# Kernel tuning notes

Measured on AMD Instinct MI355X. Metric: run time of the kernel, lower is better.

## Reference

```python
import jax, jax.numpy as jnp
import numpy as np

DIM = 512
HEADS = 8
DHEAD = 64
B, H, W = 4, 128, 128


def _dwconv(x, k):
    # x: (b, c, h, w), k: (c, 1, 3, 3) depthwise kernel (groups = c)
    return jax.lax.conv_general_dilated(
        x, k, window_strides=(1, 1), padding='SAME',
        dimension_numbers=('NCHW', 'OIHW', 'NCHW'),
        feature_group_count=x.shape[1])


def _l2norm(x, eps=1e-12):
    # torch F.normalize(p=2, dim=-1): x / clamp(||x||, eps)
    n = jnp.sqrt(jnp.sum(x * x, axis=-1, keepdims=True))
    return x / jnp.maximum(n, eps)


def setup_inputs() -> dict:
    key = jax.random.key(0)
    ks = jax.random.split(key, 10)
    s = 0.02
    return {
        'x_in': jax.random.normal(ks[0], (B, H, W, DIM), jnp.float32),
        'illu_fea_trans': jax.random.uniform(ks[1], (B, H, W, DIM), jnp.float32),
        'Wq': jax.random.normal(ks[2], (DIM, DIM), jnp.float32) * s,  # (out,in), no bias
        'Wk': jax.random.normal(ks[3], (DIM, DIM), jnp.float32) * s,
        'Wv': jax.random.normal(ks[4], (DIM, DIM), jnp.float32) * s,
        'rescale': jnp.ones((HEADS, 1, 1), jnp.float32),
        'Wp': jax.random.normal(ks[5], (DIM, DIM), jnp.float32) * s,  # proj weight (out,in)
        'bp': jnp.zeros((DIM,), jnp.float32),
        'pe1': jax.random.normal(ks[6], (DIM, 1, 3, 3), jnp.float32) * s,  # depthwise conv kernels
        'pe2': jax.random.normal(ks[7], (DIM, 1, 3, 3), jnp.float32) * s,
    }


def reference(x_in, illu_fea_trans, Wq, Wk, Wv, rescale, Wp, bp, pe1, pe2):
    b, h, w, c = x_in.shape
    n = h * w
    x = x_in.reshape(b, n, c)
    illu = illu_fea_trans.reshape(b, n, c)

    q = x @ Wq.T
    k = x @ Wk.T
    v = x @ Wv.T

    def to_heads_dn(t):  # (b, n, heads*d) -> (b, heads, d, n)
        return t.reshape(b, n, HEADS, DHEAD).transpose(0, 2, 3, 1)

    illu_h = illu.reshape(b, n, HEADS, DHEAD)
    v = ((v.reshape(b, n, HEADS, DHEAD)) * illu_h).transpose(0, 2, 3, 1)  # (b,heads,d,n)
    q = _l2norm(to_heads_dn(q))  # normalize along n
    k = _l2norm(to_heads_dn(k))

    # channel attention: (b,heads,d,d) score matrix
    attn = jnp.einsum('bhdn,bhen->bhde', k, q) * rescale
    attn = jax.nn.softmax(attn, axis=-1)
    xo = jnp.einsum('bhde,bhen->bhdn', attn, v)  # (b,heads,d,n)

    xo = xo.transpose(0, 3, 1, 2).reshape(b, n, HEADS * DHEAD)  # (b,n,c)
    out_c = (xo @ Wp.T + bp).reshape(b, h, w, c)

    # positional branch: depthwise conv -> GELU -> depthwise conv on v image
    v_img = v.reshape(b, HEADS * DHEAD, h, w)
    p = _dwconv(v_img, pe1)
    p = jax.nn.gelu(p, approximate=False)  # torch F.gelu default = erf
    p = _dwconv(p, pe2)
    out_p = p.transpose(0, 2, 3, 1)

    return out_c + out_p
```

## Files before the change

kernel.cpp:

```cpp
#include <hip/hip_runtime.h>
#include <hip/hip_bf16.h>
#include <math.h>

typedef __bf16 bf16;
typedef __attribute__((ext_vector_type(8))) __bf16 bf16x8;
typedef __attribute__((ext_vector_type(4))) float f32x4;

#define GLL(gp, lp) __builtin_amdgcn_global_load_lds( \
    (const __attribute__((address_space(1))) unsigned int*)(gp), \
    (__attribute__((address_space(3))) unsigned int*)(lp), 16, 0, 0)


__device__ __forceinline__ bf16x8 cvt8(float4 a, float4 b) {
  bf16x8 o;
  o[0] = (bf16)a.x; o[1] = (bf16)a.y; o[2] = (bf16)a.z; o[3] = (bf16)a.w;
  o[4] = (bf16)b.x; o[5] = (bf16)b.y; o[6] = (bf16)b.z; o[7] = (bf16)b.w;
  return o;
}

__global__ __launch_bounds__(256) void prep_kernel(
    const float* __restrict__ x, const float* __restrict__ Wq,
    const float* __restrict__ Wk, const float* __restrict__ Wv,
    bf16* __restrict__ xb, bf16* __restrict__ wqkv,
    float* __restrict__ zattn, float* __restrict__ ssq, float* __restrict__ ssk)
{
  const long XG = 33554432L / 8;
  const long WG = 262144L / 8;
  long i = (long)blockIdx.x * 256 + threadIdx.x;
  if (i < XG) {
    const float4* xp = (const float4*)x;
    float4 a = xp[i * 2], b = xp[i * 2 + 1];
    *(bf16x8*)(xb + i * 8) = cvt8(a, b);
  } else if (i < XG + 3 * WG) {
    long j = i - XG;
    int w = (int)(j / WG);
    long r = j % WG;
    const float* src = (w == 0) ? Wq : ((w == 1) ? Wk : Wv);
    const float4* sp = (const float4*)src;
    float4 a = sp[r * 2], b = sp[r * 2 + 1];
    *(bf16x8*)(wqkv + (long)w * 262144 + r * 8) = cvt8(a, b);
  } else {
    long j = (i - XG - 3 * WG) * 8;
    float4 z = make_float4(0.f, 0.f, 0.f, 0.f);
    if (j < 131072) {
      *(float4*)(zattn + j) = z; *(float4*)(zattn + j + 4) = z;
    } else if (j < 133120) {
      long r = j - 131072; *(float4*)(ssq + r) = z; *(float4*)(ssq + r + 4) = z;
    } else {
      long r = j - 133120; *(float4*)(ssk + r) = z; *(float4*)(ssk + r + 4) = z;
    }
  }
}

__device__ __forceinline__ void gemm_tile_mainloop(
    const bf16* __restrict__ A, const bf16* __restrict__ B,
    int m0, int n0, bf16* As, bf16* Bs, f32x4 acc[4][4])
{
  int tid = threadIdx.x;
  int lane = tid & 63, wave = tid >> 6;
  int wy = wave >> 1, wx = wave & 1;
  int srow = tid >> 3;
  int scol = ((tid & 7) ^ (srow & 7)) * 8;
  const bf16* ag = A + ((size_t)(m0 + srow) << 9) + scol;
  const bf16* bg = B + ((size_t)(n0 + srow) << 9) + scol;
  bf16* lA = As + wave * 512;
  bf16* lB = Bs + wave * 512;
  int mloc = lane & 15;
  int kq = lane >> 4;

#pragma unroll
  for (int i = 0; i < 4; i++) {
    GLL(ag + i * 16384, lA + i * 2048);
    GLL(bg + i * 16384, lB + i * 2048);
  }
  __syncthreads();

#pragma unroll
  for (int k0 = 0; k0 < 512; k0 += 64) {
    int cur = (k0 >> 6) & 1;
    if (k0 + 64 < 512) {
      int nb = cur ^ 1;
#pragma unroll
      for (int i = 0; i < 4; i++) {
        GLL(ag + (k0 + 64) + i * 16384, lA + nb * 8192 + i * 2048);
        GLL(bg + (k0 + 64) + i * 16384, lB + nb * 8192 + i * 2048);
      }
    }
    const bf16* Ac = As + (cur << 13);
    const bf16* Bc = Bs + (cur << 13);
#pragma unroll
    for (int kh = 0; kh < 2; kh++) {
      bf16x8 af[4], bfr[4];
      int logical = kh * 4 + kq;
#pragma unroll
      for (int tt = 0; tt < 4; tt++) {
        int arow = wy * 64 + tt * 16 + mloc;
        af[tt] = *(const bf16x8*)&Ac[arow * 64 + (logical ^ (arow & 7)) * 8];
        int brow = wx * 64 + tt * 16 + mloc;
        bfr[tt] = *(const bf16x8*)&Bc[brow * 64 + (logical ^ (brow & 7)) * 8];
      }
#pragma unroll
      for (int ty = 0; ty < 4; ty++)
#pragma unroll
        for (int tx = 0; tx < 4; tx++)
          acc[ty][tx] = __builtin_amdgcn_mfma_f32_16x16x32_bf16(
              af[ty], bfr[tx], acc[ty][tx], 0, 0, 0);
    }
    __syncthreads();
  }
}

__global__ __launch_bounds__(256) void gemm_qkv_kernel(
    const bf16* __restrict__ xb, const bf16* __restrict__ wqkv,
    const float* __restrict__ illu,
    bf16* __restrict__ qb, bf16* __restrict__ kb, bf16* __restrict__ vb,
    float* __restrict__ ssq, float* __restrict__ ssk)
{
  __shared__ __align__(16) bf16 As[16384];
  __shared__ __align__(16) bf16 Bs[16384];
  int bid = blockIdx.x;
  int xcd = bid & 7, s = bid >> 3;
  int mt = xcd * 64 + s / 12, nt = s % 12;
  int m0 = mt * 128, n0 = nt * 128;
  f32x4 acc[4][4] = {};
  gemm_tile_mainloop(xb, wqkv, m0, n0, As, Bs, acc);

  int tid = threadIdx.x, lane = tid & 63, wave = tid >> 6;
  int wy = wave >> 1, wx = wave & 1;
  int r0 = m0 + wy * 64 + ((lane >> 4) << 2);
  int c0 = n0 + wx * 64 + (lane & 15);
  int region = n0 >> 9;
  if (region < 2) {
    bf16* outp = region ? kb : qb;
    float* dst = (region ? ssk : ssq) + (m0 >> 14) * 512;
#pragma unroll
    for (int tx = 0; tx < 4; tx++) {
      int lc = (c0 + tx * 16) & 511;
      float ss = 0.f;
#pragma unroll
      for (int ty = 0; ty < 4; ty++) {
#pragma unroll
        for (int r = 0; r < 4; r++) {
          float v = acc[ty][tx][r];
          ss += v * v;
          outp[((size_t)(r0 + ty * 16 + r) << 9) + lc] = (bf16)v;
        }
      }
      ss += __shfl_xor(ss, 16);
      ss += __shfl_xor(ss, 32);
      if ((lane >> 4) == 0) atomicAdd(dst + lc, ss);
    }
  } else {
#pragma unroll
    for (int tx = 0; tx < 4; tx++) {
      int lc = (c0 + tx * 16) & 511;
#pragma unroll
      for (int ty = 0; ty < 4; ty++) {
#pragma unroll
        for (int r = 0; r < 4; r++) {
          size_t idx = ((size_t)(r0 + ty * 16 + r) << 9) + lc;
          vb[idx] = (bf16)(acc[ty][tx][r] * illu[idx]);
        }
      }
    }
  }
}

__global__ __launch_bounds__(256) void attn_dots_kernel(
    const bf16* __restrict__ qb, const bf16* __restrict__ kb,
    float* __restrict__ attn)
{
  __shared__ __align__(16) float ks[32 * 68];
  __shared__ __align__(16) float qs[32 * 68];
  int bh = blockIdx.x, sp = blockIdx.y;
  int b = bh >> 3, h = bh & 7;
  size_t hb = ((size_t)b << 23) + (size_t)h * 64;
  const bf16* qp = qb + hb;
  const bf16* kp = kb + hb;
  int t = threadIdx.x;
  int srow = t >> 3, scg = (t & 7) * 8;
  int d0 = (t & 15) * 4, e0 = (t >> 4) * 4;
  float acc[16] = {0};
  int nb = sp * 1024;
  for (int c = 0; c < 1024; c += 32) {
    size_t off = ((size_t)(nb + c + srow) << 9) + scg;
    bf16x8 kv = *(const bf16x8*)(kp + off);
    bf16x8 qv = *(const bf16x8*)(qp + off);
    __syncthreads();
    float* kd = &ks[srow * 68 + scg];
    float* qd = &qs[srow * 68 + scg];
#pragma unroll
    for (int i = 0; i < 8; i++) { kd[i] = (float)kv[i]; qd[i] = (float)qv[i]; }
    __syncthreads();
#pragma unroll 8
    for (int n = 0; n < 32; n++) {
      float4 kr = *(const float4*)&ks[n * 68 + d0];
      float4 qr = *(const float4*)&qs[n * 68 + e0];
      acc[0]  += kr.x * qr.x; acc[1]  += kr.x * qr.y; acc[2]  += kr.x * qr.z; acc[3]  += kr.x * qr.w;
      acc[4]  += kr.y * qr.x; acc[5]  += kr.y * qr.y; acc[6]  += kr.y * qr.z; acc[7]  += kr.y * qr.w;
      acc[8]  += kr.z * qr.x; acc[9]  += kr.z * qr.y; acc[10] += kr.z * qr.z; acc[11] += kr.z * qr.w;
      acc[12] += kr.w * qr.x; acc[13] += kr.w * qr.y; acc[14] += kr.w * qr.z; acc[15] += kr.w * qr.w;
    }
  }
  float* ap = attn + ((size_t)bh << 12);
#pragma unroll
  for (int i = 0; i < 4; i++)
#pragma unroll
    for (int j = 0; j < 4; j++)
      atomicAdd(&ap[(d0 + i) * 64 + (e0 + j)], acc[i * 4 + j]);
}

__global__ __launch_bounds__(64) void softmax_kernel(
    float* __restrict__ attn, const float* __restrict__ ssq,
    const float* __restrict__ ssk, const float* __restrict__ rescale)
{
  int bh = blockIdx.x, d = blockIdx.y;
  int b = bh >> 3, h = bh & 7;
  int e = threadIdx.x;
  float nq = fmaxf(sqrtf(ssq[b * 512 + h * 64 + e]), 1e-12f);
  float nk = fmaxf(sqrtf(ssk[b * 512 + h * 64 + d]), 1e-12f);
  float* ap = attn + ((size_t)bh << 12) + d * 64;
  float v = ap[e] * rescale[h] / (nk * nq);
  float m = v;
  for (int o = 32; o > 0; o >>= 1) m = fmaxf(m, __shfl_xor(m, o));
  float ex = expf(v - m);
  float s = ex;
  for (int o = 32; o > 0; o >>= 1) s += __shfl_xor(s, o);
  ap[e] = ex / s;
}

__global__ __launch_bounds__(256) void weff_kernel(
    const float* __restrict__ attn, const float* __restrict__ Wp,
    bf16* __restrict__ wefT)
{
  int cog = blockIdx.x, h = blockIdx.y, b = blockIdx.z;
  __shared__ float at[4096];
  __shared__ float wp[4096];
  int t = threadIdx.x;
  const float* ap = attn + ((size_t)(b * 8 + h) << 12);
  for (int i = t; i < 4096; i += 256) at[i] = ap[i];
  for (int i = t; i < 4096; i += 256) {
    int r = i >> 6, d = i & 63;
    wp[i] = Wp[((size_t)(cog * 64 + r) << 9) + h * 64 + d];
  }
  __syncthreads();
  int co_l = (t & 15) * 4, e_l = (t >> 4) * 4;
  float acc[16] = {0};
  for (int d = 0; d < 64; d++) {
    float w0 = wp[(co_l + 0) * 64 + d];
    float w1 = wp[(co_l + 1) * 64 + d];
    float w2 = wp[(co_l + 2) * 64 + d];
    float w3 = wp[(co_l + 3) * 64 + d];
    float4 av = *(const float4*)&at[d * 64 + e_l];
    acc[0]  += w0 * av.x; acc[1]  += w0 * av.y; acc[2]  += w0 * av.z; acc[3]  += w0 * av.w;
    acc[4]  += w1 * av.x; acc[5]  += w1 * av.y; acc[6]  += w1 * av.z; acc[7]  += w1 * av.w;
    acc[8]  += w2 * av.x; acc[9]  += w2 * av.y; acc[10] += w2 * av.z; acc[11] += w2 * av.w;
    acc[12] += w3 * av.x; acc[13] += w3 * av.y; acc[14] += w3 * av.z; acc[15] += w3 * av.w;
  }
#pragma unroll
  for (int i = 0; i < 4; i++)
#pragma unroll
    for (int j = 0; j < 4; j++)
      wefT[((size_t)b << 18) + ((size_t)(cog * 64 + co_l + i) << 9) + h * 64 + e_l + j] =
          (bf16)acc[i * 4 + j];
}

__global__ __launch_bounds__(256) void gemm_out_kernel(
    const bf16* __restrict__ vb, const bf16* __restrict__ wefT,
    const float* __restrict__ bp, float* __restrict__ out)
{
  __shared__ __align__(16) bf16 As[16384];
  __shared__ __align__(16) bf16 Bs[16384];
  int b = blockIdx.y;
  int bid = blockIdx.x;
  int xcd = bid & 7, s = bid >> 3;
  int mt = xcd * 16 + (s >> 2), nt = s & 3;
  int m0 = mt * 128, n0 = nt * 128;
  const bf16* A = vb + ((size_t)b << 23);
  const bf16* B = wefT + ((size_t)b << 18);
  f32x4 acc[4][4] = {};
  gemm_tile_mainloop(A, B, m0, n0, As, Bs, acc);

  int tid = threadIdx.x, lane = tid & 63, wave = tid >> 6;
  int wy = wave >> 1, wx = wave & 1;
  int r0 = (b << 14) + m0 + wy * 64 + ((lane >> 4) << 2);
  int c0 = n0 + wx * 64 + (lane & 15);
#pragma unroll
  for (int ty = 0; ty < 4; ty++) {
#pragma unroll
    for (int tx = 0; tx < 4; tx++) {
      int lc = c0 + tx * 16;
      float bias = bp[lc];
#pragma unroll
      for (int r = 0; r < 4; r++) {
        int grow = r0 + ty * 16 + r;
        out[((size_t)grow << 9) + lc] = acc[ty][tx][r] + bias;
      }
    }
  }
}

__global__ __launch_bounds__(256) void conv1_kernel(
    const bf16* __restrict__ vb, const float* __restrict__ pe1,
    bf16* __restrict__ pbuf)
{
  int b = blockIdx.y;
  int tile = blockIdx.x;
  int y0 = (tile >> 4) * 8, x0 = (tile & 15) * 8;
  int t = threadIdx.x;
  int cg = (t & 63) * 8, sp0 = t >> 6;
  float w[72];
#pragma unroll
  for (int i = 0; i < 8; i++)
#pragma unroll
    for (int k = 0; k < 9; k++)
      w[i * 9 + k] = pe1[(cg + i) * 9 + k];
  const bf16* vbase = vb + ((size_t)b << 23);
  bf16* pb = pbuf + ((size_t)b << 23);
  for (int s = sp0; s < 64; s += 4) {
    int y = y0 + (s >> 3), x = x0 + (s & 7);
    float a[8] = {0, 0, 0, 0, 0, 0, 0, 0};
#pragma unroll
    for (int ky = 0; ky < 3; ky++) {
      int yy = y + ky - 1;
      if (yy < 0 || yy >= 128) continue;
#pragma unroll
      for (int kx = 0; kx < 3; kx++) {
        int xx = x + kx - 1;
        if (xx < 0 || xx >= 128) continue;
        bf16x8 vv = *(const bf16x8*)&vbase[((size_t)(yy * 128 + xx) << 9) + cg];
#pragma unroll
        for (int i = 0; i < 8; i++) a[i] += (float)vv[i] * w[i * 9 + ky * 3 + kx];
      }
    }
    bf16x8 o;
#pragma unroll
    for (int i = 0; i < 8; i++) {
      float g = 0.5f * a[i] * (1.0f + erff(a[i] * 0.70710678118654752f));
      o[i] = (bf16)g;
    }
    *(bf16x8*)&pb[((size_t)(y * 128 + x) << 9) + cg] = o;
  }
}

__global__ __launch_bounds__(256) void conv2_kernel(
    const bf16* __restrict__ pbuf, const float* __restrict__ pe2,
    float* __restrict__ out)
{
  int b = blockIdx.y;
  int tile = blockIdx.x;
  int y0 = (tile >> 4) * 8, x0 = (tile & 15) * 8;
  int t = threadIdx.x;
  int cg = (t & 63) * 8, sp0 = t >> 6;
  float w[72];
#pragma unroll
  for (int i = 0; i < 8; i++)
#pragma unroll
    for (int k = 0; k < 9; k++)
      w[i * 9 + k] = pe2[(cg + i) * 9 + k];
  const bf16* pb = pbuf + ((size_t)b << 23);
  float* ob = out + ((size_t)b << 23);
  for (int s = sp0; s < 64; s += 4) {
    int y = y0 + (s >> 3), x = x0 + (s & 7);
    float a[8] = {0, 0, 0, 0, 0, 0, 0, 0};
#pragma unroll
    for (int ky = 0; ky < 3; ky++) {
      int yy = y + ky - 1;
      if (yy < 0 || yy >= 128) continue;
#pragma unroll
      for (int kx = 0; kx < 3; kx++) {
        int xx = x + kx - 1;
        if (xx < 0 || xx >= 128) continue;
        bf16x8 vv = *(const bf16x8*)&pb[((size_t)(yy * 128 + xx) << 9) + cg];
#pragma unroll
        for (int i = 0; i < 8; i++) a[i] += (float)vv[i] * w[i * 9 + ky * 3 + kx];
      }
    }
    size_t oi = ((size_t)(y * 128 + x) << 9) + cg;
    float4 o0 = *(float4*)&ob[oi];
    float4 o1 = *(float4*)&ob[oi + 4];
    o0.x += a[0]; o0.y += a[1]; o0.z += a[2]; o0.w += a[3];
    o1.x += a[4]; o1.y += a[5]; o1.z += a[6]; o1.w += a[7];
    *(float4*)&ob[oi] = o0;
    *(float4*)&ob[oi + 4] = o1;
  }
}

extern "C" void kernel_launch(void* const* d_in, const int* in_sizes, int n_in,
                              void* d_out, int out_size, void* d_ws, size_t ws_size,
                              hipStream_t stream) {
  (void)in_sizes; (void)n_in; (void)out_size; (void)ws_size;
  const float* x       = (const float*)d_in[0];
  const float* illu    = (const float*)d_in[1];
  const float* Wq      = (const float*)d_in[2];
  const float* Wk      = (const float*)d_in[3];
  const float* Wv      = (const float*)d_in[4];
  const float* rescale = (const float*)d_in[5];
  const float* Wp      = (const float*)d_in[6];
  const float* bp      = (const float*)d_in[7];
  const float* pe1     = (const float*)d_in[8];
  const float* pe2     = (const float*)d_in[9];
  float* out = (float*)d_out;
  char* ws = (char*)d_ws;

  bf16*  xb   = (bf16*)(ws);
  bf16*  wqkv = (bf16*)(ws + 67108864);
  bf16*  qb   = (bf16*)(ws + 68681728);
  bf16*  kb   = (bf16*)(ws + 135790592);
  bf16*  vb   = (bf16*)(ws + 202899456);
  float* ssq  = (float*)(ws + 270008320);
  float* ssk  = (float*)(ws + 270016512);
  float* attn = (float*)(ws + 270024704);
  bf16*  wefT = (bf16*)(ws + 270548992);
  bf16*  pbuf = xb;

  prep_kernel<<<16834, 256, 0, stream>>>(x, Wq, Wk, Wv, xb, wqkv, attn, ssq, ssk);
  gemm_qkv_kernel<<<6144, 256, 0, stream>>>(xb, wqkv, illu, qb, kb, vb, ssq, ssk);
  attn_dots_kernel<<<dim3(32, 16), 256, 0, stream>>>(qb, kb, attn);
  softmax_kernel<<<dim3(32, 64), 64, 0, stream>>>(attn, ssq, ssk, rescale);
  weff_kernel<<<dim3(8, 8, 4), 256, 0, stream>>>(attn, Wp, wefT);
  gemm_out_kernel<<<dim3(512, 4), 256, 0, stream>>>(vb, wefT, bp, out);
  conv1_kernel<<<dim3(256, 4), 256, 0, stream>>>(vb, pe1, pbuf);
  conv2_kernel<<<dim3(256, 4), 256, 0, stream>>>(pbuf, pe2, out);
}
```

Baseline: 838.3 us.

## Use 256x256 GEMM tiles with 8 waves and phased explicit-wait pipelining

Both bf16 GEMMs (QKV projection and output projection) move from 128x128 tiles with 4 waves to 256x256 tiles with 8 waves per block. The main loop is rewritten into four compute phases per k-step, with staggered global-to-LDS loads, explicit vmcnt/lgkmcnt waits, raw s_barrier and setprio around the MFMA bursts. The aim is higher arithmetic intensity per LDS byte and better overlap of loads with MFMA. In exchange LDS use per block doubles to 128KB, and register pressure rises to 32 accumulators per thread, which may limit occupancy or cause spills.

Result: slower. 940.6 us (+12.2%).

```diff
diff --git a/kernel.cpp b/kernel.cpp
--- a/kernel.cpp
+++ b/kernel.cpp
@@ -9,6 +9,12 @@
 #define GLL(gp, lp) __builtin_amdgcn_global_load_lds( \
     (const __attribute__((address_space(1))) unsigned int*)(gp), \
     (__attribute__((address_space(3))) unsigned int*)(lp), 16, 0, 0)
+
+#define S_BARRIER() __builtin_amdgcn_s_barrier()
+#define WAIT_LGKM0() do { asm volatile("s_waitcnt lgkmcnt(0)" ::: "memory"); \
+                          __builtin_amdgcn_sched_barrier(0); } while (0)
+#define WAIT_VMC(n) do { asm volatile("s_waitcnt vmcnt(" #n ")" ::: "memory"); \
+                         __builtin_amdgcn_sched_barrier(0); } while (0)
 
 
 __device__ __forceinline__ bf16x8 cvt8(float4 a, float4 b) {
@@ -52,98 +58,125 @@
   }
 }
 
-__device__ __forceinline__ void gemm_tile_mainloop(
+__device__ __forceinline__ void gemm256_mainloop(
     const bf16* __restrict__ A, const bf16* __restrict__ B,
-    int m0, int n0, bf16* As, bf16* Bs, f32x4 acc[4][4])
-{
-  int tid = threadIdx.x;
-  int lane = tid & 63, wave = tid >> 6;
-  int wy = wave >> 1, wx = wave & 1;
-  int srow = tid >> 3;
-  int scol = ((tid & 7) ^ (srow & 7)) * 8;
+    int m0, int n0, bf16* As, bf16* Bs, f32x4 (&acc)[8][4])
+{
+  const int tid = threadIdx.x;
+  const int lane = tid & 63, wave = tid >> 6;
+  const int wy = wave >> 2, wx = wave & 3;
+  const int srow = tid >> 3;
+  const int scol = ((tid & 7) ^ (srow & 7)) * 8;
   const bf16* ag = A + ((size_t)(m0 + srow) << 9) + scol;
   const bf16* bg = B + ((size_t)(n0 + srow) << 9) + scol;
   bf16* lA = As + wave * 512;
   bf16* lB = Bs + wave * 512;
-  int mloc = lane & 15;
-  int kq = lane >> 4;
-
-#pragma unroll
-  for (int i = 0; i < 4; i++) {
-    GLL(ag + i * 16384, lA + i * 2048);
-    GLL(bg + i * 16384, lB + i * 2048);
-  }
-  __syncthreads();
-
-#pragma unroll
-  for (int k0 = 0; k0 < 512; k0 += 64) {
-    int cur = (k0 >> 6) & 1;
-    if (k0 + 64 < 512) {
-      int nb = cur ^ 1;
-#pragma unroll
-      for (int i = 0; i < 4; i++) {
-        GLL(ag + (k0 + 64) + i * 16384, lA + nb * 8192 + i * 2048);
-        GLL(bg + (k0 + 64) + i * 16384, lB + nb * 8192 + i * 2048);
-      }
-    }
-    const bf16* Ac = As + (cur << 13);
-    const bf16* Bc = Bs + (cur << 13);
-#pragma unroll
-    for (int kh = 0; kh < 2; kh++) {
-      bf16x8 af[4], bfr[4];
-      int logical = kh * 4 + kq;
-#pragma unroll
-      for (int tt = 0; tt < 4; tt++) {
-        int arow = wy * 64 + tt * 16 + mloc;
-        af[tt] = *(const bf16x8*)&Ac[arow * 64 + (logical ^ (arow & 7)) * 8];
-        int brow = wx * 64 + tt * 16 + mloc;
-        bfr[tt] = *(const bf16x8*)&Bc[brow * 64 + (logical ^ (brow & 7)) * 8];
-      }
-#pragma unroll
-      for (int ty = 0; ty < 4; ty++)
-#pragma unroll
-        for (int tx = 0; tx < 4; tx++)
-          acc[ty][tx] = __builtin_amdgcn_mfma_f32_16x16x32_bf16(
-              af[ty], bfr[tx], acc[ty][tx], 0, 0, 0);
-    }
-    __syncthreads();
-  }
-}
-
-__global__ __launch_bounds__(256) void gemm_qkv_kernel(
+  const int mloc = lane & 15, kq = lane >> 4;
+
+#define STG_A(t, i) GLL(ag + (size_t)(i) * 32768 + (t) * 64, \
+                        lA + (((t) & 1) * 16384 + (i) * 4096))
+#define STG_B(t, i) GLL(bg + (size_t)(i) * 32768 + (t) * 64, \
+                        lB + (((t) & 1) * 16384 + (i) * 4096))
+
+#pragma unroll
+  for (int i = 0; i < 4; ++i) STG_A(0, i);
+#pragma unroll
+  for (int i = 0; i < 4; ++i) STG_B(0, i);
+#pragma unroll
+  for (int i = 0; i < 4; ++i) STG_B(1, i);
+  WAIT_VMC(4);
+  S_BARRIER();
+
+  bf16x8 af[4][2];
+  bf16x8 bfr[2][2][2];
+
+#pragma unroll
+  for (int kt = 0; kt < 8; ++kt) {
+    const int s = kt & 1;
+#pragma unroll
+    for (int ph = 0; ph < 4; ++ph) {
+      const int rh = ph >> 1, ch = ph & 1;
+      if (ch == 0) {
+#pragma unroll
+        for (int rt = 0; rt < 4; ++rt) {
+          const int r = wy * 128 + rh * 64 + rt * 16 + mloc;
+#pragma unroll
+          for (int kh = 0; kh < 2; ++kh)
+            af[rt][kh] = *(const bf16x8*)
+                &As[s * 16384 + r * 64 + (((kh * 4 + kq) ^ (r & 7)) << 3)];
+        }
+      }
+      if (ph < 2) {
+#pragma unroll
+        for (int ct = 0; ct < 2; ++ct) {
+          const int nr = wx * 64 + ch * 32 + ct * 16 + mloc;
+#pragma unroll
+          for (int kh = 0; kh < 2; ++kh)
+            bfr[ch][ct][kh] = *(const bf16x8*)
+                &Bs[s * 16384 + nr * 64 + (((kh * 4 + kq) ^ (nr & 7)) << 3)];
+        }
+      }
+      if (ph == 0 && kt + 1 < 8) { STG_A(kt + 1, 0); STG_A(kt + 1, 1); }
+      if (ph == 1 && kt + 1 < 8) { STG_A(kt + 1, 2); STG_A(kt + 1, 3); }
+      if (ph == 2 && kt + 2 < 8) { STG_B(kt + 2, 0); STG_B(kt + 2, 1); }
+      if (ph == 3 && kt + 2 < 8) { STG_B(kt + 2, 2); STG_B(kt + 2, 3); }
+      if (ph == 3) {
+        if (kt <= 5)      { WAIT_VMC(4); }
+        else if (kt == 6) { WAIT_VMC(0); }
+      }
+      S_BARRIER();
+      WAIT_LGKM0();
+      __builtin_amdgcn_s_setprio(1);
+#pragma unroll
+      for (int rt = 0; rt < 4; ++rt)
+#pragma unroll
+        for (int ct = 0; ct < 2; ++ct)
+#pragma unroll
+          for (int kh = 0; kh < 2; ++kh)
+            acc[rh * 4 + rt][ch * 2 + ct] = __builtin_amdgcn_mfma_f32_16x16x32_bf16(
+                af[rt][kh], bfr[ch][ct][kh], acc[rh * 4 + rt][ch * 2 + ct], 0, 0, 0);
+      __builtin_amdgcn_s_setprio(0);
+      S_BARRIER();
+    }
+  }
+#undef STG_A
+#undef STG_B
+}
+
+__global__ __launch_bounds__(512, 2) void gemm_qkv_kernel(
     const bf16* __restrict__ xb, const bf16* __restrict__ wqkv,
     const float* __restrict__ illu,
     bf16* __restrict__ qb, bf16* __restrict__ kb, bf16* __restrict__ vb,
     float* __restrict__ ssq, float* __restrict__ ssk)
 {
-  __shared__ __align__(16) bf16 As[16384];
-  __shared__ __align__(16) bf16 Bs[16384];
+  __shared__ __align__(16) bf16 As[32768];
+  __shared__ __align__(16) bf16 Bs[32768];
   int bid = blockIdx.x;
   int xcd = bid & 7, s = bid >> 3;
-  int mt = xcd * 64 + s / 12, nt = s % 12;
-  int m0 = mt * 128, n0 = nt * 128;
-  f32x4 acc[4][4] = {};
-  gemm_tile_mainloop(xb, wqkv, m0, n0, As, Bs, acc);
+  int mt = xcd * 32 + s / 6, nt = s % 6;
+  int m0 = mt * 256, n0 = nt * 256;
+  f32x4 acc[8][4] = {};
+  gemm256_mainloop(xb, wqkv, m0, n0, As, Bs, acc);
 
   int tid = threadIdx.x, lane = tid & 63, wave = tid >> 6;
-  int wy = wave >> 1, wx = wave & 1;
-  int r0 = m0 + wy * 64 + ((lane >> 4) << 2);
+  int wy = wave >> 2, wx = wave & 3;
+  int r0 = m0 + wy * 128 + ((lane >> 4) << 2);
   int c0 = n0 + wx * 64 + (lane & 15);
   int region = n0 >> 9;
   if (region < 2) {
     bf16* outp = region ? kb : qb;
     float* dst = (region ? ssk : ssq) + (m0 >> 14) * 512;
 #pragma unroll
-    for (int tx = 0; tx < 4; tx++) {
-      int lc = (c0 + tx * 16) & 511;
+    for (int tj = 0; tj < 4; ++tj) {
+      int lc = (c0 + tj * 16) & 511;
       float ss = 0.f;
 #pragma unroll
-      for (int ty = 0; ty < 4; ty++) {
-#pragma unroll
-        for (int r = 0; r < 4; r++) {
-          float v = acc[ty][tx][r];
+      for (int ti = 0; ti < 8; ++ti) {
+#pragma unroll
+        for (int r = 0; r < 4; ++r) {
+          float v = acc[ti][tj][r];
           ss += v * v;
-          outp[((size_t)(r0 + ty * 16 + r) << 9) + lc] = (bf16)v;
+          outp[((size_t)(r0 + ti * 16 + r) << 9) + lc] = (bf16)v;
         }
       }
       ss += __shfl_xor(ss, 16);
@@ -152,14 +185,14 @@
     }
   } else {
 #pragma unroll
-    for (int tx = 0; tx < 4; tx++) {
-      int lc = (c0 + tx * 16) & 511;
-#pragma unroll
-      for (int ty = 0; ty < 4; ty++) {
-#pragma unroll
-        for (int r = 0; r < 4; r++) {
-          size_t idx = ((size_t)(r0 + ty * 16 + r) << 9) + lc;
-          vb[idx] = (bf16)(acc[ty][tx][r] * illu[idx]);
+    for (int tj = 0; tj < 4; ++tj) {
+      int lc = (c0 + tj * 16) & 511;
+#pragma unroll
+      for (int ti = 0; ti < 8; ++ti) {
+#pragma unroll
+        for (int r = 0; r < 4; ++r) {
+          size_t idx = ((size_t)(r0 + ti * 16 + r) << 9) + lc;
+          vb[idx] = (bf16)(acc[ti][tj][r] * illu[idx]);
         }
       }
     }
@@ -265,36 +298,36 @@
           (bf16)acc[i * 4 + j];
 }
 
-__global__ __launch_bounds__(256) void gemm_out_kernel(
+__global__ __launch_bounds__(512, 2) void gemm_out_kernel(
     const bf16* __restrict__ vb, const bf16* __restrict__ wefT,
     const float* __restrict__ bp, float* __restrict__ out)
 {
-  __shared__ __align__(16) bf16 As[16384];
-  __shared__ __align__(16) bf16 Bs[16384];
+  __shared__ __align__(16) bf16 As[32768];
+  __shared__ __align__(16) bf16 Bs[32768];
   int b = blockIdx.y;
   int bid = blockIdx.x;
   int xcd = bid & 7, s = bid >> 3;
-  int mt = xcd * 16 + (s >> 2), nt = s & 3;
-  int m0 = mt * 128, n0 = nt * 128;
+  int mt = xcd * 8 + (s >> 1), nt = s & 1;
+  int m0 = mt * 256, n0 = nt * 256;
   const bf16* A = vb + ((size_t)b << 23);
   const bf16* B = wefT + ((size_t)b << 18);
-  f32x4 acc[4][4] = {};
-  gemm_tile_mainloop(A, B, m0, n0, As, Bs, acc);
+  f32x4 acc[8][4] = {};
+  gemm256_mainloop(A, B, m0, n0, As, Bs, acc);
 
   int tid = threadIdx.x, lane = tid & 63, wave = tid >> 6;
-  int wy = wave >> 1, wx = wave & 1;
-  int r0 = (b << 14) + m0 + wy * 64 + ((lane >> 4) << 2);
+  int wy = wave >> 2, wx = wave & 3;
+  int r0 = (b << 14) + m0 + wy * 128 + ((lane >> 4) << 2);
   int c0 = n0 + wx * 64 + (lane & 15);
 #pragma unroll
-  for (int ty = 0; ty < 4; ty++) {
-#pragma unroll
-    for (int tx = 0; tx < 4; tx++) {
-      int lc = c0 + tx * 16;
+  for (int ti = 0; ti < 8; ++ti) {
+#pragma unroll
+    for (int tj = 0; tj < 4; ++tj) {
+      int lc = c0 + tj * 16;
       float bias = bp[lc];
 #pragma unroll
-      for (int r = 0; r < 4; r++) {
-        int grow = r0 + ty * 16 + r;
-        out[((size_t)grow << 9) + lc] = acc[ty][tx][r] + bias;
+      for (int r = 0; r < 4; ++r) {
+        int grow = r0 + ti * 16 + r;
+        out[((size_t)grow << 9) + lc] = acc[ti][tj][r] + bias;
       }
     }
   }
@@ -415,11 +448,11 @@
   bf16*  pbuf = xb;
 
   prep_kernel<<<16834, 256, 0, stream>>>(x, Wq, Wk, Wv, xb, wqkv, attn, ssq, ssk);
-  gemm_qkv_kernel<<<6144, 256, 0, stream>>>(xb, wqkv, illu, qb, kb, vb, ssq, ssk);
+  gemm_qkv_kernel<<<1536, 512, 0, stream>>>(xb, wqkv, illu, qb, kb, vb, ssq, ssk);
   attn_dots_kernel<<<dim3(32, 16), 256, 0, stream>>>(qb, kb, attn);
   softmax_kernel<<<dim3(32, 64), 64, 0, stream>>>(attn, ssq, ssk, rescale);
   weff_kernel<<<dim3(8, 8, 4), 256, 0, stream>>>(attn, Wp, wefT);
-  gemm_out_kernel<<<dim3(512, 4), 256, 0, stream>>>(vb, wefT, bp, out);
+  gemm_out_kernel<<<dim3(128, 4), 512, 0, stream>>>(vb, wefT, bp, out);
   conv1_kernel<<<dim3(256, 4), 256, 0, stream>>>(vb, pe1, pbuf);
   conv2_kernel<<<dim3(256, 4), 256, 0, stream>>>(pbuf, pe2, out);
 }
```

## Store Q/K transposed and compute channel-attention dots with MFMA

Applied to the files above, without the earlier changes.

The QKV GEMM epilogue now writes Q and K in a channel-major (transposed) layout with 4-wide vector stores along n. The attn_dots kernel then streams contiguous n-chunks straight into swizzled LDS via global_load_lds and computes the 64x64 K·Q^T products with bf16 MFMA, each wave taking its own n slice, instead of scalar FP32 FMAs over LDS tiles. This removes the bf16-to-float conversion and the scalar inner loop, at the cost of more atomicAdds per block (one per wave) and strided transposed stores in the GEMM epilogue.

Result: faster. 810.7 us (-3.3%).

```diff
diff --git a/kernel.cpp b/kernel.cpp
--- a/kernel.cpp
+++ b/kernel.cpp
@@ -3,12 +3,18 @@
 #include <math.h>
 
 typedef __bf16 bf16;
+typedef __attribute__((ext_vector_type(4))) __bf16 bf16x4;
 typedef __attribute__((ext_vector_type(8))) __bf16 bf16x8;
 typedef __attribute__((ext_vector_type(4))) float f32x4;
 
 #define GLL(gp, lp) __builtin_amdgcn_global_load_lds( \
     (const __attribute__((address_space(1))) unsigned int*)(gp), \
     (__attribute__((address_space(3))) unsigned int*)(lp), 16, 0, 0)
+
+#define WAIT_LGKM0() do { asm volatile("s_waitcnt lgkmcnt(0)" ::: "memory"); \
+                          __builtin_amdgcn_sched_barrier(0); } while (0)
+#define WAIT_VMC0() do { asm volatile("s_waitcnt vmcnt(0)" ::: "memory"); \
+                         __builtin_amdgcn_sched_barrier(0); } while (0)
 
 
 __device__ __forceinline__ bf16x8 cvt8(float4 a, float4 b) {
@@ -113,7 +119,7 @@
 __global__ __launch_bounds__(256) void gemm_qkv_kernel(
     const bf16* __restrict__ xb, const bf16* __restrict__ wqkv,
     const float* __restrict__ illu,
-    bf16* __restrict__ qb, bf16* __restrict__ kb, bf16* __restrict__ vb,
+    bf16* __restrict__ qbT, bf16* __restrict__ kbT, bf16* __restrict__ vb,
     float* __restrict__ ssq, float* __restrict__ ssk)
 {
   __shared__ __align__(16) bf16 As[16384];
@@ -131,20 +137,22 @@
   int c0 = n0 + wx * 64 + (lane & 15);
   int region = n0 >> 9;
   if (region < 2) {
-    bf16* outp = region ? kb : qb;
+    bf16* outp = region ? kbT : qbT;
     float* dst = (region ? ssk : ssq) + (m0 >> 14) * 512;
+    int bb = r0 >> 14;
+    int nl0 = r0 & 16383;
 #pragma unroll
     for (int tx = 0; tx < 4; tx++) {
       int lc = (c0 + tx * 16) & 511;
+      bf16* colp = outp + (((size_t)bb << 23) + ((size_t)lc << 14));
       float ss = 0.f;
 #pragma unroll
       for (int ty = 0; ty < 4; ty++) {
-#pragma unroll
-        for (int r = 0; r < 4; r++) {
-          float v = acc[ty][tx][r];
-          ss += v * v;
-          outp[((size_t)(r0 + ty * 16 + r) << 9) + lc] = (bf16)v;
-        }
+        f32x4 a = acc[ty][tx];
+        ss += a[0] * a[0] + a[1] * a[1] + a[2] * a[2] + a[3] * a[3];
+        bf16x4 o;
+        o[0] = (bf16)a[0]; o[1] = (bf16)a[1]; o[2] = (bf16)a[2]; o[3] = (bf16)a[3];
+        *(bf16x4*)&colp[nl0 + ty * 16] = o;
       }
       ss += __shfl_xor(ss, 16);
       ss += __shfl_xor(ss, 32);
@@ -167,47 +175,62 @@
 }
 
 __global__ __launch_bounds__(256) void attn_dots_kernel(
-    const bf16* __restrict__ qb, const bf16* __restrict__ kb,
+    const bf16* __restrict__ qbT, const bf16* __restrict__ kbT,
     float* __restrict__ attn)
 {
-  __shared__ __align__(16) float ks[32 * 68];
-  __shared__ __align__(16) float qs[32 * 68];
+  __shared__ __align__(16) bf16 ks[4][4096];
+  __shared__ __align__(16) bf16 qs[4][4096];
   int bh = blockIdx.x, sp = blockIdx.y;
   int b = bh >> 3, h = bh & 7;
-  size_t hb = ((size_t)b << 23) + (size_t)h * 64;
-  const bf16* qp = qb + hb;
-  const bf16* kp = kb + hb;
-  int t = threadIdx.x;
-  int srow = t >> 3, scg = (t & 7) * 8;
-  int d0 = (t & 15) * 4, e0 = (t >> 4) * 4;
-  float acc[16] = {0};
-  int nb = sp * 1024;
-  for (int c = 0; c < 1024; c += 32) {
-    size_t off = ((size_t)(nb + c + srow) << 9) + scg;
-    bf16x8 kv = *(const bf16x8*)(kp + off);
-    bf16x8 qv = *(const bf16x8*)(qp + off);
-    __syncthreads();
-    float* kd = &ks[srow * 68 + scg];
-    float* qd = &qs[srow * 68 + scg];
-#pragma unroll
-    for (int i = 0; i < 8; i++) { kd[i] = (float)kv[i]; qd[i] = (float)qv[i]; }
-    __syncthreads();
-#pragma unroll 8
-    for (int n = 0; n < 32; n++) {
-      float4 kr = *(const float4*)&ks[n * 68 + d0];
-      float4 qr = *(const float4*)&qs[n * 68 + e0];
-      acc[0]  += kr.x * qr.x; acc[1]  += kr.x * qr.y; acc[2]  += kr.x * qr.z; acc[3]  += kr.x * qr.w;
-      acc[4]  += kr.y * qr.x; acc[5]  += kr.y * qr.y; acc[6]  += kr.y * qr.z; acc[7]  += kr.y * qr.w;
-      acc[8]  += kr.z * qr.x; acc[9]  += kr.z * qr.y; acc[10] += kr.z * qr.z; acc[11] += kr.z * qr.w;
-      acc[12] += kr.w * qr.x; acc[13] += kr.w * qr.y; acc[14] += kr.w * qr.z; acc[15] += kr.w * qr.w;
-    }
+  int t = threadIdx.x, lane = t & 63, w = t >> 6;
+  size_t base = ((size_t)b << 23) + ((size_t)h << 20);
+  int n0 = sp * 1024 + w * 256;
+  int srow = lane >> 3;
+  int scol = ((lane & 7) ^ (srow & 7)) << 3;
+  const bf16* kg = kbT + base + (size_t)srow * 16384 + n0 + scol;
+  const bf16* qg = qbT + base + (size_t)srow * 16384 + n0 + scol;
+  bf16* lk = &ks[w][0];
+  bf16* lq = &qs[w][0];
+  int mloc = lane & 15, kq = lane >> 4;
+  f32x4 acc[4][4] = {};
+
+  for (int it = 0; it < 4; ++it) {
+    WAIT_LGKM0();
+#pragma unroll
+    for (int i = 0; i < 8; ++i) {
+      GLL(kg + it * 64 + (size_t)i * 131072, lk + i * 512);
+      GLL(qg + it * 64 + (size_t)i * 131072, lq + i * 512);
+    }
+    WAIT_VMC0();
+    bf16x8 af[4][2], bfq[4][2];
+#pragma unroll
+    for (int tt = 0; tt < 4; ++tt) {
+      int r = tt * 16 + mloc;
+#pragma unroll
+      for (int kh = 0; kh < 2; ++kh) {
+        int slot = (kh * 4 + kq) ^ (r & 7);
+        af[tt][kh]  = *(const bf16x8*)&lk[r * 64 + slot * 8];
+        bfq[tt][kh] = *(const bf16x8*)&lq[r * 64 + slot * 8];
+      }
+    }
+#pragma unroll
+    for (int kh = 0; kh < 2; ++kh)
+#pragma unroll
+      for (int ta = 0; ta < 4; ++ta)
+#pragma unroll
+        for (int tb = 0; tb < 4; ++tb)
+          acc[ta][tb] = __builtin_amdgcn_mfma_f32_16x16x32_bf16(
+              af[ta][kh], bfq[tb][kh], acc[ta][tb], 0, 0, 0);
   }
   float* ap = attn + ((size_t)bh << 12);
-#pragma unroll
-  for (int i = 0; i < 4; i++)
-#pragma unroll
-    for (int j = 0; j < 4; j++)
-      atomicAdd(&ap[(d0 + i) * 64 + (e0 + j)], acc[i * 4 + j]);
+  int rr = (lane >> 4) << 2, cc = lane & 15;
+#pragma unroll
+  for (int ta = 0; ta < 4; ++ta)
+#pragma unroll
+    for (int tb = 0; tb < 4; ++tb)
+#pragma unroll
+      for (int r = 0; r < 4; ++r)
+        atomicAdd(&ap[(ta * 16 + rr + r) * 64 + tb * 16 + cc], acc[ta][tb][r]);
 }
 
 __global__ __launch_bounds__(64) void softmax_kernel(
@@ -405,8 +428,8 @@
 
   bf16*  xb   = (bf16*)(ws);
   bf16*  wqkv = (bf16*)(ws + 67108864);
-  bf16*  qb   = (bf16*)(ws + 68681728);
-  bf16*  kb   = (bf16*)(ws + 135790592);
+  bf16*  qbT  = (bf16*)(ws + 68681728);
+  bf16*  kbT  = (bf16*)(ws + 135790592);
   bf16*  vb   = (bf16*)(ws + 202899456);
   float* ssq  = (float*)(ws + 270008320);
   float* ssk  = (float*)(ws + 270016512);
@@ -415,8 +438,8 @@
   bf16*  pbuf = xb;
 
   prep_kernel<<<16834, 256, 0, stream>>>(x, Wq, Wk, Wv, xb, wqkv, attn, ssq, ssk);
-  gemm_qkv_kernel<<<6144, 256, 0, stream>>>(xb, wqkv, illu, qb, kb, vb, ssq, ssk);
-  attn_dots_kernel<<<dim3(32, 16), 256, 0, stream>>>(qb, kb, attn);
+  gemm_qkv_kernel<<<6144, 256, 0, stream>>>(xb, wqkv, illu, qbT, kbT, vb, ssq, ssk);
+  attn_dots_kernel<<<dim3(32, 16), 256, 0, stream>>>(qbT, kbT, attn);
   softmax_kernel<<<dim3(32, 64), 64, 0, stream>>>(attn, ssq, ssk, rescale);
   weff_kernel<<<dim3(8, 8, 4), 256, 0, stream>>>(attn, Wp, wefT);
   gemm_out_kernel<<<dim3(512, 4), 256, 0, stream>>>(vb, wefT, bp, out);
```
